# Performance work log

Measured on AMD Instinct MI355X. Metric: run time of the kernel, lower is better.

## Reference

```python
import jax, jax.numpy as jnp
import numpy as np
from jax import lax

B, T, I, H = 4096, 64, 8, 128


def _lstm_layer(xs, W_ih, W_hh, b):
    # xs: [T, B, D_in]; PyTorch gate order i, f, g, o
    def step(carry, x_t):
        h, c = carry
        gates = x_t @ W_ih.T + h @ W_hh.T + b  # [B, 4H]
        i, f, g, o = jnp.split(gates, 4, axis=-1)
        i = jax.nn.sigmoid(i)
        f = jax.nn.sigmoid(f)
        g = jnp.tanh(g)
        o = jax.nn.sigmoid(o)
        c_new = f * c + i * g
        h_new = o * jnp.tanh(c_new)
        return (h_new, c_new), h_new

    n_b = xs.shape[1]
    h0 = jnp.zeros((n_b, W_hh.shape[1]), xs.dtype)
    c0 = jnp.zeros((n_b, W_hh.shape[1]), xs.dtype)
    (h_last, _), ys = lax.scan(step, (h0, c0), xs)
    return ys, h_last


def setup_inputs() -> dict:
    key = jax.random.key(0)
    ks = jax.random.split(key, 14)
    s = 1.0 / np.sqrt(H)
    u = lambda k, shape: jax.random.uniform(k, shape, jnp.float32, -s, s)
    return {
        "x": jax.random.normal(ks[0], (B, T, I), jnp.float32),
        "W_ih0": u(ks[1], (4 * H, I)),
        "W_hh0": u(ks[2], (4 * H, H)),
        "b_ih0": u(ks[3], (4 * H,)),
        "b_hh0": u(ks[4], (4 * H,)),
        "W_ih1": u(ks[5], (4 * H, H)),
        "W_hh1": u(ks[6], (4 * H, H)),
        "b_ih1": u(ks[7], (4 * H,)),
        "b_hh1": u(ks[8], (4 * H,)),
        "W_d1": u(ks[9], (5, H)),
        "b_d1": u(ks[10], (5,)),
        "W_d2": u(ks[11], (1, 5)),
        "b_d2": u(ks[12], (1,)),
    }


def reference(x, W_ih0, W_hh0, b_ih0, b_hh0, W_ih1, W_hh1, b_ih1, b_hh1,
              W_d1, b_d1, W_d2, b_d2):
    xs = jnp.transpose(x, (1, 0, 2))  # [T, B, I]
    ys0, _ = _lstm_layer(xs, W_ih0, W_hh0, b_ih0 + b_hh0)
    # inter-layer dropout (p=0.2) and trailing Dropout are identity in eval mode
    _, h_last = _lstm_layer(ys0, W_ih1, W_hh1, b_ih1 + b_hh1)  # [B, H]
    out = jax.nn.relu(h_last)
    out = jax.nn.relu(out @ W_d1.T + b_d1)  # [B, 5]
    out = out @ W_d2.T + b_d2  # [B, 1]
    return out
```

## Files before the change

### kernel.cpp

```cpp
#include <hip/hip_runtime.h>

typedef _Float16 h8 __attribute__((ext_vector_type(8)));
typedef _Float16 h4 __attribute__((ext_vector_type(4)));
typedef float f4 __attribute__((ext_vector_type(4)));
typedef int i4v __attribute__((ext_vector_type(4)));

#define B_ 4096
#define T_ 64
#define I_ 8
#define H_ 128

#define WC0_OFF 0
#define H0_OFF  131072
#define H1_OFF  139264
#define BB_OFF  147456
#define LDS_TOTAL 149504

#define LOG2E    1.4426950408889634f
#define TWOLOG2E 2.8853900817779268f

__device__ __forceinline__ float sigm2_(float v) {
    return __builtin_amdgcn_rcpf(1.f + exp2f(-v));
}
__device__ __forceinline__ float tanh2_(float v) {
    return 1.f - 2.f * __builtin_amdgcn_rcpf(exp2f(v) + 1.f);
}
__device__ __forceinline__ float tanhn_(float v) {
    return 1.f - 2.f * __builtin_amdgcn_rcpf(exp2f(TWOLOG2E * v) + 1.f);
}
__device__ __forceinline__ int gs_of(int p) {
    return (p & 3) * H_ + (p >> 6) * 16 + ((p >> 2) & 3) * 4 + ((p >> 4) & 3);
}
__device__ __forceinline__ float scl_(int q) { return (q == 2) ? TWOLOG2E : LOG2E; }

__device__ __forceinline__ int ag_w(int v) {
    int r; asm volatile("v_accvgpr_write_b32 %0, %1" : "=a"(r) : "v"(v)); return r;
}
__device__ __forceinline__ int ag_r(int v) {
    int r; asm volatile("v_accvgpr_read_b32 %0, %1" : "=v"(r) : "a"(v)); return r;
}

__global__ __launch_bounds__(512) void lstm_fused_kernel(
    const float* __restrict__ x,
    const float* __restrict__ Wih0, const float* __restrict__ Whh0,
    const float* __restrict__ bih0, const float* __restrict__ bhh0,
    const float* __restrict__ Wih1, const float* __restrict__ Whh1,
    const float* __restrict__ bih1, const float* __restrict__ bhh1,
    const float* __restrict__ Wd1, const float* __restrict__ bd1,
    const float* __restrict__ Wd2, const float* __restrict__ bd2,
    float* __restrict__ out)
{
    __shared__ __align__(16) unsigned char lds[LDS_TOTAL];
    const int tid = threadIdx.x;
    const int w   = tid >> 6;
    const int l   = tid & 63;
    const int c16 = l & 15;
    const int G4  = l >> 4;
    const int rowbase = blockIdx.x * 16;
    const int swzl = c16 << 4;

    {
        const int p  = tid;
        const int gs = gs_of(p);
        const float sc = scl_(p & 3);
        const float* src = Whh0 + (size_t)gs * H_;
        const int swz = (p & 15) << 4;
        unsigned char* dst = lds + WC0_OFF + p * 256;
#pragma unroll
        for (int kb = 0; kb < 16; kb++) {
            float4 f0 = *(const float4*)(src + kb * 8);
            float4 f1 = *(const float4*)(src + kb * 8 + 4);
            h8 v;
            v[0]=(_Float16)(f0.x*sc); v[1]=(_Float16)(f0.y*sc);
            v[2]=(_Float16)(f0.z*sc); v[3]=(_Float16)(f0.w*sc);
            v[4]=(_Float16)(f1.x*sc); v[5]=(_Float16)(f1.y*sc);
            v[6]=(_Float16)(f1.z*sc); v[7]=(_Float16)(f1.w*sc);
            *(h8*)(dst + ((kb * 16) ^ swz)) = v;
        }
    }
    {
        f4 z = {0.f, 0.f, 0.f, 0.f};
        if (tid < 256) *(f4*)(lds + H0_OFF + 4096 + tid * 16) = z;
        else           *(f4*)(lds + H1_OFF + 4096 + (tid - 256) * 16) = z;
        const int gs = gs_of(tid);
        ((float*)(lds + BB_OFF))[tid] = (bih1[gs] + bhh1[gs]) * scl_(tid & 3);
    }

    int wag[96];
    h8 wc1v[4][2];
    h4 ax16[4];
    {
        const float sc1 = scl_(c16 & 3);
#pragma unroll
        for (int j = 0; j < 4; j++) {
            const int gs = gs_of(w * 64 + j * 16 + c16);
#pragma unroll
            for (int ks = 0; ks < 8; ks++) {
                const int k0 = ks * 32 + G4 * 8;
                const float* src = (k0 < 128) ? (Whh1 + (size_t)gs * H_ + k0)
                                              : (Wih1 + (size_t)gs * H_ + (k0 - 128));
                float4 f0 = *(const float4*)src;
                float4 f1 = *(const float4*)(src + 4);
                h8 v;
                v[0]=(_Float16)(f0.x*sc1); v[1]=(_Float16)(f0.y*sc1);
                v[2]=(_Float16)(f0.z*sc1); v[3]=(_Float16)(f0.w*sc1);
                v[4]=(_Float16)(f1.x*sc1); v[5]=(_Float16)(f1.y*sc1);
                v[6]=(_Float16)(f1.z*sc1); v[7]=(_Float16)(f1.w*sc1);
                if (ks < 6) {
                    i4v iv = *(i4v*)&v;
                    wag[(j * 6 + ks) * 4 + 0] = ag_w(iv[0]);
                    wag[(j * 6 + ks) * 4 + 1] = ag_w(iv[1]);
                    wag[(j * 6 + ks) * 4 + 2] = ag_w(iv[2]);
                    wag[(j * 6 + ks) * 4 + 3] = ag_w(iv[3]);
                } else {
                    wc1v[j][ks - 6] = v;
                }
            }
            h4 a;
#pragma unroll
            for (int e = 0; e < 4; e++) {
                const int k = G4 * 4 + e;
                float val = 0.f;
                if (k < 8)       val = Wih0[(size_t)gs * I_ + k] * sc1;
                else if (k == 8) val = (bih0[gs] + bhh0[gs]) * sc1;
                a[e] = (_Float16)val;
            }
            ax16[j] = a;
        }
    }

    const float* xrow = x + (size_t)(rowbase + c16) * T_ * I_;
    float4 xf0 = *(const float4*)(xrow);
    float4 xf1 = *(const float4*)(xrow + 4);

    float c0r[4] = {0.f, 0.f, 0.f, 0.f};
    float c1r[4] = {0.f, 0.f, 0.f, 0.f};

    __syncthreads();

    int cur = 0;
    for (int t = 0; t < T_; t++) {
        h4 bx;
        bx[0] = (_Float16)0.f; bx[1] = (_Float16)0.f;
        bx[2] = (_Float16)0.f; bx[3] = (_Float16)0.f;
        if (G4 == 0) {
            bx[0]=(_Float16)xf0.x; bx[1]=(_Float16)xf0.y;
            bx[2]=(_Float16)xf0.z; bx[3]=(_Float16)xf0.w;
        } else if (G4 == 1) {
            bx[0]=(_Float16)xf1.x; bx[1]=(_Float16)xf1.y;
            bx[2]=(_Float16)xf1.z; bx[3]=(_Float16)xf1.w;
        } else if (G4 == 2) {
            bx[0] = (_Float16)1.f;
        }
        if (t < T_ - 1) {
            xf0 = *(const float4*)(xrow + (t + 1) * 8);
            xf1 = *(const float4*)(xrow + (t + 1) * 8 + 4);
        }

        f4 acc0[4], acc1[4];
        {
            f4 z = {0.f, 0.f, 0.f, 0.f};
#pragma unroll
            for (int j = 0; j < 4; j++) acc0[j] = z;
        }
        const unsigned char* h0rd = lds + H0_OFF + (cur ^ 1) * 4096;
#pragma unroll
        for (int ks = 0; ks < 4; ks++) {
            h8 b = *(const h8*)(h0rd + ((c16 * 256 + ks * 64 + G4 * 16) ^ swzl));
#pragma unroll
            for (int j = 0; j < 4; j++) {
                h8 a = *(const h8*)(lds + WC0_OFF + (w * 64 + j * 16 + c16) * 256
                                    + ((ks * 64 + G4 * 16) ^ swzl));
                acc0[j] = __builtin_amdgcn_mfma_f32_16x16x32_f16(a, b, acc0[j], 0, 0, 0);
            }
        }
#pragma unroll
        for (int j = 0; j < 4; j++)
            acc0[j] = __builtin_amdgcn_mfma_f32_16x16x16f16(ax16[j], bx, acc0[j], 0, 0, 0);

        const unsigned char* h1rd = lds + H1_OFF + (cur ^ 1) * 4096;
#pragma unroll
        for (int j = 0; j < 4; j++)
            acc1[j] = *(const f4*)(lds + BB_OFF + (w * 64 + j * 16 + G4 * 4) * 4);
#pragma unroll
        for (int ks = 0; ks < 4; ks++) {
            h8 b = *(const h8*)(h1rd + ((c16 * 256 + ks * 64 + G4 * 16) ^ swzl));
#pragma unroll
            for (int j = 0; j < 4; j++) {
                i4v iv;
                iv[0] = ag_r(wag[(j * 6 + ks) * 4 + 0]);
                iv[1] = ag_r(wag[(j * 6 + ks) * 4 + 1]);
                iv[2] = ag_r(wag[(j * 6 + ks) * 4 + 2]);
                iv[3] = ag_r(wag[(j * 6 + ks) * 4 + 3]);
                h8 a = *(h8*)&iv;
                acc1[j] = __builtin_amdgcn_mfma_f32_16x16x32_f16(a, b, acc1[j], 0, 0, 0);
            }
        }

        unsigned char* h0wr = lds + H0_OFF + cur * 4096;
        {
            h4 hv;
#pragma unroll
            for (int j = 0; j < 4; j++) {
                const float vi = sigm2_(acc0[j][0]);
                const float vf = sigm2_(acc0[j][1]);
                const float vg = tanh2_(acc0[j][2]);
                const float vo = sigm2_(acc0[j][3]);
                const float cn = vf * c0r[j] + vi * vg;
                c0r[j] = cn;
                hv[j] = (_Float16)(vo * tanhn_(cn));
            }
            *(h4*)(h0wr + ((c16 * 256 + w * 32 + G4 * 8) ^ swzl)) = hv;
        }

        __syncthreads();

        const unsigned char* h0n = lds + H0_OFF + cur * 4096;
#pragma unroll
        for (int ks = 0; ks < 4; ks++) {
            h8 b = *(const h8*)(h0n + ((c16 * 256 + ks * 64 + G4 * 16) ^ swzl));
#pragma unroll
            for (int j = 0; j < 4; j++) {
                h8 a;
                if (ks < 2) {
                    i4v iv;
                    iv[0] = ag_r(wag[(j * 6 + 4 + ks) * 4 + 0]);
                    iv[1] = ag_r(wag[(j * 6 + 4 + ks) * 4 + 1]);
                    iv[2] = ag_r(wag[(j * 6 + 4 + ks) * 4 + 2]);
                    iv[3] = ag_r(wag[(j * 6 + 4 + ks) * 4 + 3]);
                    a = *(h8*)&iv;
                } else {
                    a = wc1v[j][ks - 2];
                }
                acc1[j] = __builtin_amdgcn_mfma_f32_16x16x32_f16(a, b, acc1[j], 0, 0, 0);
            }
        }
        unsigned char* h1wr = lds + H1_OFF + cur * 4096;
        {
            h4 hv;
#pragma unroll
            for (int j = 0; j < 4; j++) {
                const float vi = sigm2_(acc1[j][0]);
                const float vf = sigm2_(acc1[j][1]);
                const float vg = tanh2_(acc1[j][2]);
                const float vo = sigm2_(acc1[j][3]);
                const float cn = vf * c1r[j] + vi * vg;
                c1r[j] = cn;
                hv[j] = (_Float16)(vo * tanhn_(cn));
            }
            *(h4*)(h1wr + ((c16 * 256 + w * 32 + G4 * 8) ^ swzl)) = hv;
        }

        __syncthreads();
        cur ^= 1;
    }

    if (tid < 128) {
        const int r = tid >> 3, part = tid & 7;
        const unsigned char* h1f = lds + H1_OFF + 4096;
        const int rswz = r << 4;
        float s0 = 0.f, s1 = 0.f, s2 = 0.f, s3 = 0.f, s4 = 0.f;
#pragma unroll
        for (int kk = 0; kk < 16; kk++) {
            const int k = part * 16 + kk;
            float a = (float)*(const _Float16*)(h1f + ((r * 256 + k * 2) ^ rswz));
            a = fmaxf(a, 0.f);
            s0 += a * Wd1[0 * H_ + k];
            s1 += a * Wd1[1 * H_ + k];
            s2 += a * Wd1[2 * H_ + k];
            s3 += a * Wd1[3 * H_ + k];
            s4 += a * Wd1[4 * H_ + k];
        }
#pragma unroll
        for (int m = 1; m < 8; m <<= 1) {
            s0 += __shfl_xor(s0, m);
            s1 += __shfl_xor(s1, m);
            s2 += __shfl_xor(s2, m);
            s3 += __shfl_xor(s3, m);
            s4 += __shfl_xor(s4, m);
        }
        if (part == 0) {
            float o = bd2[0];
            o += fmaxf(s0 + bd1[0], 0.f) * Wd2[0];
            o += fmaxf(s1 + bd1[1], 0.f) * Wd2[1];
            o += fmaxf(s2 + bd1[2], 0.f) * Wd2[2];
            o += fmaxf(s3 + bd1[3], 0.f) * Wd2[3];
            o += fmaxf(s4 + bd1[4], 0.f) * Wd2[4];
            out[rowbase + r] = o;
        }
    }
}

extern "C" void kernel_launch(void* const* d_in, const int* in_sizes, int n_in,
                              void* d_out, int out_size, void* d_ws, size_t ws_size,
                              hipStream_t stream)
{
    const float* x    = (const float*)d_in[0];
    const float* Wih0 = (const float*)d_in[1];
    const float* Whh0 = (const float*)d_in[2];
    const float* bih0 = (const float*)d_in[3];
    const float* bhh0 = (const float*)d_in[4];
    const float* Wih1 = (const float*)d_in[5];
    const float* Whh1 = (const float*)d_in[6];
    const float* bih1 = (const float*)d_in[7];
    const float* bhh1 = (const float*)d_in[8];
    const float* Wd1  = (const float*)d_in[9];
    const float* bd1  = (const float*)d_in[10];
    const float* Wd2  = (const float*)d_in[11];
    const float* bd2  = (const float*)d_in[12];

    lstm_fused_kernel<<<B_ / 16, 512, 0, stream>>>(
        x, Wih0, Whh0, bih0, bhh0, Wih1, Whh1, bih1, bhh1,
        Wd1, bd1, Wd2, bd2, (float*)d_out);
}
```

Baseline: 225.7 us.

## Skew layer-1 LSTM one step behind layer 0 to halve barriers

Restructures the time loop so layer 1 at step t-1 runs in the same iteration as layer 0 at step t, both reading the layer-0 hidden state written in the previous iteration. This removes one __syncthreads per step and lets the two layers' MFMA chains interleave, at the cost of one extra loop iteration. All of layer 1's weights now sit in AGPRs (wag grows to 128), and the layer-1 bias is kept as fp16 registers added before the activations instead of an LDS-initialised accumulator. Risks are higher register pressure and a small precision loss from rounding the bias to fp16.

```diff
diff --git a/kernel.cpp b/kernel.cpp
--- a/kernel.cpp
+++ b/kernel.cpp
@@ -13,8 +13,7 @@
 #define WC0_OFF 0
 #define H0_OFF  131072
 #define H1_OFF  139264
-#define BB_OFF  147456
-#define LDS_TOTAL 149504
+#define LDS_TOTAL 147456
 
 #define LOG2E    1.4426950408889634f
 #define TWOLOG2E 2.8853900817779268f
@@ -82,13 +81,11 @@
         f4 z = {0.f, 0.f, 0.f, 0.f};
         if (tid < 256) *(f4*)(lds + H0_OFF + 4096 + tid * 16) = z;
         else           *(f4*)(lds + H1_OFF + 4096 + (tid - 256) * 16) = z;
-        const int gs = gs_of(tid);
-        ((float*)(lds + BB_OFF))[tid] = (bih1[gs] + bhh1[gs]) * scl_(tid & 3);
-    }
-
-    int wag[96];
-    h8 wc1v[4][2];
+    }
+
+    int wag[128];
     h4 ax16[4];
+    h4 b1h[4];
     {
         const float sc1 = scl_(c16 & 3);
 #pragma unroll
@@ -106,15 +103,11 @@
                 v[2]=(_Float16)(f0.z*sc1); v[3]=(_Float16)(f0.w*sc1);
                 v[4]=(_Float16)(f1.x*sc1); v[5]=(_Float16)(f1.y*sc1);
                 v[6]=(_Float16)(f1.z*sc1); v[7]=(_Float16)(f1.w*sc1);
-                if (ks < 6) {
-                    i4v iv = *(i4v*)&v;
-                    wag[(j * 6 + ks) * 4 + 0] = ag_w(iv[0]);
-                    wag[(j * 6 + ks) * 4 + 1] = ag_w(iv[1]);
-                    wag[(j * 6 + ks) * 4 + 2] = ag_w(iv[2]);
-                    wag[(j * 6 + ks) * 4 + 3] = ag_w(iv[3]);
-                } else {
-                    wc1v[j][ks - 6] = v;
-                }
+                i4v iv = *(i4v*)&v;
+                wag[(j * 8 + ks) * 4 + 0] = ag_w(iv[0]);
+                wag[(j * 8 + ks) * 4 + 1] = ag_w(iv[1]);
+                wag[(j * 8 + ks) * 4 + 2] = ag_w(iv[2]);
+                wag[(j * 8 + ks) * 4 + 3] = ag_w(iv[3]);
             }
             h4 a;
 #pragma unroll
@@ -126,6 +119,11 @@
                 a[e] = (_Float16)val;
             }
             ax16[j] = a;
+#pragma unroll
+            for (int q2 = 0; q2 < 4; q2++) {
+                const int gs2 = q2 * H_ + w * 16 + G4 * 4 + j;
+                b1h[j][q2] = (_Float16)((bih1[gs2] + bhh1[gs2]) * scl_(q2));
+            }
         }
     }
 
@@ -139,7 +137,22 @@
     __syncthreads();
 
     int cur = 0;
-    for (int t = 0; t < T_; t++) {
+    for (int t = 0; t <= T_; t++) {
+        const bool doL0 = (t < T_);
+        const bool doL1 = (t > 0);
+
+        h8 b0[4], b1f[4];
+        const unsigned char* h0rd = lds + H0_OFF + (cur ^ 1) * 4096;
+#pragma unroll
+        for (int ks = 0; ks < 4; ks++)
+            b0[ks] = *(const h8*)(h0rd + ((c16 * 256 + ks * 64 + G4 * 16) ^ swzl));
+        if (doL1) {
+            const unsigned char* h1rd = lds + H1_OFF + cur * 4096;
+#pragma unroll
+            for (int ks = 0; ks < 4; ks++)
+                b1f[ks] = *(const h8*)(h1rd + ((c16 * 256 + ks * 64 + G4 * 16) ^ swzl));
+        }
+
         h4 bx;
         bx[0] = (_Float16)0.f; bx[1] = (_Float16)0.f;
         bx[2] = (_Float16)0.f; bx[3] = (_Float16)0.f;
@@ -158,47 +171,62 @@
         }
 
         f4 acc0[4], acc1[4];
-        {
-            f4 z = {0.f, 0.f, 0.f, 0.f};
-#pragma unroll
-            for (int j = 0; j < 4; j++) acc0[j] = z;
-        }
-        const unsigned char* h0rd = lds + H0_OFF + (cur ^ 1) * 4096;
-#pragma unroll
-        for (int ks = 0; ks < 4; ks++) {
-            h8 b = *(const h8*)(h0rd + ((c16 * 256 + ks * 64 + G4 * 16) ^ swzl));
-#pragma unroll
-            for (int j = 0; j < 4; j++) {
-                h8 a = *(const h8*)(lds + WC0_OFF + (w * 64 + j * 16 + c16) * 256
-                                    + ((ks * 64 + G4 * 16) ^ swzl));
-                acc0[j] = __builtin_amdgcn_mfma_f32_16x16x32_f16(a, b, acc0[j], 0, 0, 0);
-            }
-        }
-#pragma unroll
-        for (int j = 0; j < 4; j++)
-            acc0[j] = __builtin_amdgcn_mfma_f32_16x16x16f16(ax16[j], bx, acc0[j], 0, 0, 0);
-
-        const unsigned char* h1rd = lds + H1_OFF + (cur ^ 1) * 4096;
-#pragma unroll
-        for (int j = 0; j < 4; j++)
-            acc1[j] = *(const f4*)(lds + BB_OFF + (w * 64 + j * 16 + G4 * 4) * 4);
-#pragma unroll
-        for (int ks = 0; ks < 4; ks++) {
-            h8 b = *(const h8*)(h1rd + ((c16 * 256 + ks * 64 + G4 * 16) ^ swzl));
-#pragma unroll
-            for (int j = 0; j < 4; j++) {
-                i4v iv;
-                iv[0] = ag_r(wag[(j * 6 + ks) * 4 + 0]);
-                iv[1] = ag_r(wag[(j * 6 + ks) * 4 + 1]);
-                iv[2] = ag_r(wag[(j * 6 + ks) * 4 + 2]);
-                iv[3] = ag_r(wag[(j * 6 + ks) * 4 + 3]);
-                h8 a = *(h8*)&iv;
-                acc1[j] = __builtin_amdgcn_mfma_f32_16x16x32_f16(a, b, acc1[j], 0, 0, 0);
-            }
-        }
-
-        unsigned char* h0wr = lds + H0_OFF + cur * 4096;
-        {
+        if (doL0) {
+            {
+                f4 z = {0.f, 0.f, 0.f, 0.f};
+#pragma unroll
+                for (int j = 0; j < 4; j++) acc0[j] = z;
+            }
+#pragma unroll
+            for (int ks = 0; ks < 4; ks++) {
+#pragma unroll
+                for (int j = 0; j < 4; j++) {
+                    h8 a = *(const h8*)(lds + WC0_OFF + (w * 64 + j * 16 + c16) * 256
+                                        + ((ks * 64 + G4 * 16) ^ swzl));
+                    acc0[j] = __builtin_amdgcn_mfma_f32_16x16x32_f16(a, b0[ks], acc0[j], 0, 0, 0);
+                }
+            }
+#pragma unroll
+            for (int j = 0; j < 4; j++)
+                acc0[j] = __builtin_amdgcn_mfma_f32_16x16x16f16(ax16[j], bx, acc0[j], 0, 0, 0);
+        }
+
+        if (doL1) {
+            {
+                f4 z = {0.f, 0.f, 0.f, 0.f};
+#pragma unroll
+                for (int j = 0; j < 4; j++) acc1[j] = z;
+            }
+#pragma unroll
+            for (int ks = 0; ks < 4; ks++) {
+#pragma unroll
+                for (int j = 0; j < 4; j++) {
+                    i4v iv;
+                    iv[0] = ag_r(wag[(j * 8 + ks) * 4 + 0]);
+                    iv[1] = ag_r(wag[(j * 8 + ks) * 4 + 1]);
+                    iv[2] = ag_r(wag[(j * 8 + ks) * 4 + 2]);
+                    iv[3] = ag_r(wag[(j * 8 + ks) * 4 + 3]);
+                    h8 a = *(h8*)&iv;
+                    acc1[j] = __builtin_amdgcn_mfma_f32_16x16x32_f16(a, b1f[ks], acc1[j], 0, 0, 0);
+                }
+            }
+#pragma unroll
+            for (int ks = 0; ks < 4; ks++) {
+#pragma unroll
+                for (int j = 0; j < 4; j++) {
+                    i4v iv;
+                    iv[0] = ag_r(wag[(j * 8 + 4 + ks) * 4 + 0]);
+                    iv[1] = ag_r(wag[(j * 8 + 4 + ks) * 4 + 1]);
+                    iv[2] = ag_r(wag[(j * 8 + 4 + ks) * 4 + 2]);
+                    iv[3] = ag_r(wag[(j * 8 + 4 + ks) * 4 + 3]);
+                    h8 a = *(h8*)&iv;
+                    acc1[j] = __builtin_amdgcn_mfma_f32_16x16x32_f16(a, b0[ks], acc1[j], 0, 0, 0);
+                }
+            }
+        }
+
+        if (doL0) {
+            unsigned char* h0wr = lds + H0_OFF + cur * 4096;
             h4 hv;
 #pragma unroll
             for (int j = 0; j < 4; j++) {
@@ -212,38 +240,15 @@
             }
             *(h4*)(h0wr + ((c16 * 256 + w * 32 + G4 * 8) ^ swzl)) = hv;
         }
-
-        __syncthreads();
-
-        const unsigned char* h0n = lds + H0_OFF + cur * 4096;
-#pragma unroll
-        for (int ks = 0; ks < 4; ks++) {
-            h8 b = *(const h8*)(h0n + ((c16 * 256 + ks * 64 + G4 * 16) ^ swzl));
+        if (doL1) {
+            unsigned char* h1wr = lds + H1_OFF + (cur ^ 1) * 4096;
+            h4 hv;
 #pragma unroll
             for (int j = 0; j < 4; j++) {
-                h8 a;
-                if (ks < 2) {
-                    i4v iv;
-                    iv[0] = ag_r(wag[(j * 6 + 4 + ks) * 4 + 0]);
-                    iv[1] = ag_r(wag[(j * 6 + 4 + ks) * 4 + 1]);
-                    iv[2] = ag_r(wag[(j * 6 + 4 + ks) * 4 + 2]);
-                    iv[3] = ag_r(wag[(j * 6 + 4 + ks) * 4 + 3]);
-                    a = *(h8*)&iv;
-                } else {
-                    a = wc1v[j][ks - 2];
-                }
-                acc1[j] = __builtin_amdgcn_mfma_f32_16x16x32_f16(a, b, acc1[j], 0, 0, 0);
-            }
-        }
-        unsigned char* h1wr = lds + H1_OFF + cur * 4096;
-        {
-            h4 hv;
-#pragma unroll
-            for (int j = 0; j < 4; j++) {
-                const float vi = sigm2_(acc1[j][0]);
-                const float vf = sigm2_(acc1[j][1]);
-                const float vg = tanh2_(acc1[j][2]);
-                const float vo = sigm2_(acc1[j][3]);
+                const float vi = sigm2_(acc1[j][0] + (float)b1h[j][0]);
+                const float vf = sigm2_(acc1[j][1] + (float)b1h[j][1]);
+                const float vg = tanh2_(acc1[j][2] + (float)b1h[j][2]);
+                const float vo = sigm2_(acc1[j][3] + (float)b1h[j][3]);
                 const float cn = vf * c1r[j] + vi * vg;
                 c1r[j] = cn;
                 hv[j] = (_Float16)(vo * tanhn_(cn));
```

After: 307.2 us. 1.36x slower.
